# Kernel optimization log

Measured on AMD Instinct MI355X. Metric: run time of the kernel, lower is better.

## Reference

```python
import jax, jax.numpy as jnp
import numpy as np

B, NV, NE = 32, 8192, 65536
SUBSTEPS = 8
DT = 0.01
K_SPRING = 1.0e4   # spring stiffness
CG_ITERS = 20      # fixed CG iterations for the implicit solve
EPS = 1e-12


def setup_inputs() -> dict:
    key = jax.random.key(0)
    k0, k1, k2, k3, k4, k5 = jax.random.split(key, 6)
    # small actuation signals per spring (rest-length modulation)
    input_action = jax.random.normal(k0, (B, NE), dtype=jnp.float32) * 0.05
    # random spring graph with guaranteed i != j
    edge_i = jax.random.randint(k1, (NE,), 0, NV, dtype=jnp.int32)
    off = jax.random.randint(k2, (NE,), 1, NV, dtype=jnp.int32)
    edge_j = ((edge_i + off) % NV).astype(jnp.int32)
    pos0 = jax.random.normal(k3, (B, NV, 3), dtype=jnp.float32) * 0.5
    vel0 = jnp.zeros((B, NV, 3), dtype=jnp.float32)
    # rest lengths near the initial configuration so the system starts close to equilibrium
    d0 = pos0[0, edge_i] - pos0[0, edge_j]
    rest_len = jnp.linalg.norm(d0, axis=-1) + 1e-2
    mass = jax.random.uniform(k4, (NV,), dtype=jnp.float32) + 0.5
    return {"input_action": input_action, "pos0": pos0, "vel0": vel0,
            "rest_len": rest_len, "mass": mass,
            "edge_i": edge_i, "edge_j": edge_j}


def _bdot(a, b):
    # per-batch inner product, keepdims for broadcasting: [B,1,1]
    return jnp.sum(a * b, axis=(1, 2), keepdims=True)


def _spring_force(pos, rest_eff, ei, ej):
    # pos: [B,NV,3], rest_eff: [B,NE]
    d = pos[:, ei] - pos[:, ej]                       # [B,NE,3]
    l = jnp.linalg.norm(d, axis=-1, keepdims=True)    # [B,NE,1]
    dirn = d / jnp.maximum(l, 1e-6)
    fe = -K_SPRING * (l - rest_eff[..., None]) * dirn # [B,NE,3]
    f = jnp.zeros_like(pos).at[:, ei].add(fe).at[:, ej].add(-fe)
    return f


def _matvec(x, mass, ei, ej):
    # A x = M x + dt^2 * k * L x  (graph Laplacian Hessian approximation)
    d = x[:, ei] - x[:, ej]
    Lx = jnp.zeros_like(x).at[:, ei].add(d).at[:, ej].add(-d)
    return mass[None, :, None] * x + (DT * DT * K_SPRING) * Lx


def _cg_solve(b, mass, ei, ej):
    x = jnp.zeros_like(b)
    r = b
    p = r
    rs = _bdot(r, r)

    def body(carry, _):
        x, r, p, rs = carry
        Ap = _matvec(p, mass, ei, ej)
        alpha = rs / (_bdot(p, Ap) + EPS)
        x = x + alpha * p
        r = r - alpha * Ap
        rs_new = _bdot(r, r)
        p = r + (rs_new / (rs + EPS)) * p
        return (x, r, p, rs_new), None

    (x, _, _, _), _ = jax.lax.scan(body, (x, r, p, rs), None, length=CG_ITERS)
    return x


def reference(input_action, pos0, vel0, rest_len, mass, edge_i, edge_j):
    gravity = jnp.array([0.0, -9.8, 0.0], dtype=pos0.dtype)
    rest_eff = rest_len[None, :] * (1.0 + input_action)  # actuated rest lengths [B,NE]
    m3 = mass[None, :, None]

    def step(carry, _):
        pos, vel = carry
        f = _spring_force(pos, rest_eff, edge_i, edge_j) + m3 * gravity
        b = m3 * vel + DT * f                  # implicit Euler RHS
        v_new = _cg_solve(b, mass, edge_i, edge_j)
        pos_new = pos + DT * v_new
        return (pos_new, v_new), pos_new

    _, traj = jax.lax.scan(step, (pos0, vel0), None, length=SUBSTEPS)
    # traj: [SUBSTEPS, B, NV, 3] -> [B, SUBSTEPS, NV, 3]
    return jnp.transpose(traj, (1, 0, 2, 3))
```

## Files before the change

### kernel.cpp

```cpp
#include <hip/hip_runtime.h>
#include <hip/hip_cooperative_groups.h>
#include <math.h>

namespace cg = cooperative_groups;

#define NVERT 8192
#define NEDGE 65536
#define NSUB 8
#define NCG 20
#define GRID 256
#define BLOCK 1024
#define DT 0.01f
#define KS 10000.0f
#define NGRP 16
#define GSIZE 16

struct Params {
  const float* action;
  const float* pos0;
  const float* vel0;
  const float* rest_len;
  const float* mass;
  const int* edge_i;
  const int* edge_j;
  float* out;
  float2* posXY;
  float*  posZ;
  float2 *QXY0, *QXY1;
  float  *QZ0,  *QZ1;
  float* rest_eff;
  int* adj_off;
  int* adjE_off;
  int* row_ptr;
  int* cursor;
  double* Pd;
  double* Gd;
  unsigned* bar;
};

union U64F2 { unsigned long long u; float2 f; };
union U32F  { unsigned u; float f; };
union U64D  { unsigned long long u; double d; };

__device__ __forceinline__ float2 ld2_dev(const float2* p) {
  U64F2 r;
  r.u = __hip_atomic_load((const unsigned long long*)p, __ATOMIC_RELAXED, __HIP_MEMORY_SCOPE_AGENT);
  return r.f;
}
__device__ __forceinline__ void st2_dev(float2* p, float2 v) {
  U64F2 r; r.f = v;
  __hip_atomic_store((unsigned long long*)p, r.u, __ATOMIC_RELAXED, __HIP_MEMORY_SCOPE_AGENT);
}
__device__ __forceinline__ float ldf_dev(const float* p) {
  U32F r;
  r.u = __hip_atomic_load((const unsigned*)p, __ATOMIC_RELAXED, __HIP_MEMORY_SCOPE_AGENT);
  return r.f;
}
__device__ __forceinline__ void stf_dev(float* p, float v) {
  U32F r; r.f = v;
  __hip_atomic_store((unsigned*)p, r.u, __ATOMIC_RELAXED, __HIP_MEMORY_SCOPE_AGENT);
}
__device__ __forceinline__ double lddbl_dev(const double* p) {
  U64D r;
  r.u = __hip_atomic_load((const unsigned long long*)p, __ATOMIC_RELAXED, __HIP_MEMORY_SCOPE_AGENT);
  return r.d;
}
__device__ __forceinline__ void stdbl_dev(double* p, double v) {
  U64D r; r.d = v;
  __hip_atomic_store((unsigned long long*)p, r.u, __ATOMIC_RELAXED, __HIP_MEMORY_SCOPE_AGENT);
}

__device__ __forceinline__ void fast_bar(unsigned* bar, unsigned ep) {
  __syncthreads();
  if (threadIdx.x == 0) {
    const unsigned g = blockIdx.x >> 4;
    const unsigned old = __hip_atomic_fetch_add(bar + g * 32, 1u,
                          __ATOMIC_RELAXED, __HIP_MEMORY_SCOPE_AGENT);
    if (old == GSIZE * ep - 1) {
      const unsigned old2 = __hip_atomic_fetch_add(bar + NGRP * 32, 1u,
                             __ATOMIC_RELAXED, __HIP_MEMORY_SCOPE_AGENT);
      if (old2 == NGRP * ep - 1) {
#pragma unroll
        for (int i = 0; i < NGRP; ++i)
          __hip_atomic_store(bar + (NGRP + 1 + i) * 32, ep,
                             __ATOMIC_RELAXED, __HIP_MEMORY_SCOPE_AGENT);
      }
    }
    while (__hip_atomic_load(bar + (NGRP + 1 + g) * 32,
                             __ATOMIC_RELAXED, __HIP_MEMORY_SCOPE_AGENT) < ep)
      __builtin_amdgcn_s_sleep(1);
  }
  __syncthreads();
}

__device__ __forceinline__ void fast_bar_red(unsigned* bar, unsigned ep,
                                             const double* Pd, double* Gd, int par,
                                             int* lflag) {
  __syncthreads();
  const unsigned g = blockIdx.x >> 4;
  if (threadIdx.x == 0) {
    const unsigned old = __hip_atomic_fetch_add(bar + g * 32, 1u,
                          __ATOMIC_RELAXED, __HIP_MEMORY_SCOPE_AGENT);
    *lflag = (old == GSIZE * ep - 1);
  }
  __syncthreads();
  if (*lflag) {
    if (threadIdx.x < 96) {
      const double* base = Pd + (size_t)par * 256 * 96 + (size_t)(g * GSIZE) * 96
                           + threadIdx.x;
      double s = 0.0;
#pragma unroll
      for (int j = 0; j < GSIZE; ++j) s += lddbl_dev(base + j * 96);
      stdbl_dev(&Gd[(size_t)par * NGRP * 96 + g * 96 + threadIdx.x], s);
    }
    __syncthreads();
    if (threadIdx.x == 0) {
      const unsigned old2 = __hip_atomic_fetch_add(bar + NGRP * 32, 1u,
                             __ATOMIC_RELAXED, __HIP_MEMORY_SCOPE_AGENT);
      if (old2 == NGRP * ep - 1) {
#pragma unroll
        for (int i = 0; i < NGRP; ++i)
          __hip_atomic_store(bar + (NGRP + 1 + i) * 32, ep,
                             __ATOMIC_RELAXED, __HIP_MEMORY_SCOPE_AGENT);
      }
    }
  }
  if (threadIdx.x == 0) {
    while (__hip_atomic_load(bar + (NGRP + 1 + g) * 32,
                             __ATOMIC_RELAXED, __HIP_MEMORY_SCOPE_AGENT) < ep)
      __builtin_amdgcn_s_sleep(1);
  }
  __syncthreads();
}

__device__ __forceinline__ void publish_store(double* Pd, int par, double d0, double d1,
                                              double d2, double* lds) {
  d0 += __shfl_down(d0, 32);
  d1 += __shfl_down(d1, 32);
  d2 += __shfl_down(d2, 32);
  const int lane = threadIdx.x & 63, w = threadIdx.x >> 6;
  if (lane < 32) {
    lds[w * 96 + lane] = d0;
    lds[w * 96 + 32 + lane] = d1;
    lds[w * 96 + 64 + lane] = d2;
  }
  __syncthreads();
  if (threadIdx.x < 96) {
    double s = 0.0;
#pragma unroll
    for (int ww = 0; ww < BLOCK / 64; ++ww) s += lds[ww * 96 + threadIdx.x];
    stdbl_dev(&Pd[(size_t)par * 256 * 96 + (size_t)blockIdx.x * 96 + threadIdx.x], s);
  }
}

__device__ __forceinline__ void reduce_small(const double* Gd, int par,
                                             double* lds_part, double* lds_acc) {
  const int tid = threadIdx.x;
  const double* base = Gd + (size_t)par * NGRP * 96;
  lds_part[tid] = lddbl_dev(base + tid);
  if (tid < NGRP * 96 - BLOCK)
    lds_part[BLOCK + tid] = lddbl_dev(base + BLOCK + tid);
  __syncthreads();
  if (tid < 96) {
    double s = 0.0;
#pragma unroll
    for (int g = 0; g < NGRP; ++g) s += lds_part[g * 96 + tid];
    lds_acc[tid] = s;
  }
  __syncthreads();
}

__global__ void __launch_bounds__(BLOCK) mass_spring_kernel(Params P) {
  cg::grid_group grid = cg::this_grid();
  __shared__ double lds_red[(BLOCK / 64) * 96];
  __shared__ double lds_part[NGRP * 96];
  __shared__ double lds_acc[96];
  __shared__ int lds_scan[BLOCK];
  __shared__ int lds_flag;

  const int tid = threadIdx.x;
  const int gtid = blockIdx.x * BLOCK + tid;
  const int b = tid & 31;
  const int v = gtid >> 5;
  const int vb = v * 32 + b;
  const int b8 = b * 8, b4 = b * 4;
  unsigned ep = 0;

  for (int i = gtid; i < NEDGE * 32; i += GRID * BLOCK) {
    const int e = i >> 5, bb = i & 31;
    P.rest_eff[e * 32 + bb] = P.rest_len[e] * (1.0f + P.action[bb * NEDGE + e]);
  }
  float3 pv, vv;
  pv.x = P.pos0[(b * NVERT + v) * 3 + 0];
  pv.y = P.pos0[(b * NVERT + v) * 3 + 1];
  pv.z = P.pos0[(b * NVERT + v) * 3 + 2];
  vv.x = P.vel0[(b * NVERT + v) * 3 + 0];
  vv.y = P.vel0[(b * NVERT + v) * 3 + 1];
  vv.z = P.vel0[(b * NVERT + v) * 3 + 2];
  st2_dev(&P.posXY[vb], make_float2(pv.x, pv.y));
  stf_dev(&P.posZ[vb], pv.z);
  if (gtid < NVERT) P.cursor[gtid] = 0;
  if (gtid < (2 * NGRP + 1) * 32) P.bar[gtid] = 0u;
  grid.sync();

  if (gtid < NEDGE) {
    atomicAdd(&P.cursor[P.edge_i[gtid]], 1);
    atomicAdd(&P.cursor[P.edge_j[gtid]], 1);
  }
  grid.sync();

  if (blockIdx.x == 0) {
    const int base = tid * (NVERT / BLOCK);
    int loc[NVERT / BLOCK];
    int sum = 0;
#pragma unroll
    for (int i = 0; i < NVERT / BLOCK; ++i) { loc[i] = P.cursor[base + i]; sum += loc[i]; }
    lds_scan[tid] = sum;
    __syncthreads();
    for (int off = 1; off < BLOCK; off <<= 1) {
      int t = 0;
      if (tid >= off) t = lds_scan[tid - off];
      __syncthreads();
      if (tid >= off) lds_scan[tid] += t;
      __syncthreads();
    }
    int run = lds_scan[tid] - sum;
#pragma unroll
    for (int i = 0; i < NVERT / BLOCK; ++i) {
      P.row_ptr[base + i] = run;
      P.cursor[base + i] = run;
      run += loc[i];
    }
    if (tid == BLOCK - 1) P.row_ptr[NVERT] = run;
  }
  grid.sync();

  if (gtid < NEDGE) {
    const int ei = P.edge_i[gtid], ej = P.edge_j[gtid];
    const int ai = atomicAdd(&P.cursor[ei], 1);
    P.adj_off[ai] = ej * 256; P.adjE_off[ai] = gtid * 128;
    const int aj = atomicAdd(&P.cursor[ej], 1);
    P.adj_off[aj] = ei * 256; P.adjE_off[aj] = gtid * 128;
  }
  grid.sync();

  const float m_v = P.mass[v];
  const int rbeg = P.row_ptr[v], rend = P.row_ptr[v + 1];
  const float degf = (float)(rend - rbeg);

  float2* qXYrd = P.QXY0; float2* qXYwr = P.QXY1;
  float*  qZrd  = P.QZ0;  float*  qZwr  = P.QZ1;
  int pub = 0;

  for (int s = 0; s < NSUB; ++s) {
    float fx = 0.f, fy = 0.f, fz = 0.f;
#pragma unroll 4
    for (int a = rbeg; a < rend; ++a) {
      const int off = P.adj_off[a];
      const float2 pxy = ld2_dev((const float2*)((const char*)P.posXY + off + b8));
      const float  puz = ldf_dev((const float*)((const char*)P.posZ + (off >> 1) + b4));
      const float re = *(const float*)((const char*)P.rest_eff + P.adjE_off[a] + b4);
      const float dx = pv.x - pxy.x, dy = pv.y - pxy.y, dz = pv.z - puz;
      const float l = sqrtf(dx * dx + dy * dy + dz * dz);
      const float coef = -KS * (l - re) / fmaxf(l, 1e-6f);
      fx += coef * dx; fy += coef * dy; fz += coef * dz;
    }
    float3 rv;
    rv.x = m_v * vv.x + DT * fx;
    rv.y = m_v * vv.y + DT * (fy - 9.8f * m_v);
    rv.z = m_v * vv.z + DT * fz;
    st2_dev(&qXYrd[vb], make_float2(rv.x, rv.y));
    stf_dev(&qZrd[vb], rv.z);
    float3 xacc = make_float3(0.f, 0.f, 0.f);
    float3 pc = rv;
    float3 ap;
    float3 Sr, Sp;
    fast_bar(P.bar, ++ep);

    for (int k = 0; k < NCG; ++k) {
      if (k == 0) {
        float sx = 0.f, sy = 0.f, sz = 0.f;
#pragma unroll 4
        for (int a = rbeg; a < rend; ++a) {
          const int off = P.adj_off[a];
          const float2 qxy = ld2_dev((const float2*)((const char*)qXYrd + off + b8));
          const float  qz  = ldf_dev((const float*)((const char*)qZrd + (off >> 1) + b4));
          sx += qxy.x; sy += qxy.y; sz += qz;
        }
        Sr = make_float3(sx, sy, sz);
        Sp = Sr;
        ap.x = (m_v + degf) * pc.x - Sp.x;
        ap.y = (m_v + degf) * pc.y - Sp.y;
        ap.z = (m_v + degf) * pc.z - Sp.z;
      } else {
        const double* gbase = P.Gd + (size_t)((pub + 1) & 1) * NGRP * 96;
        const double gval0 = lddbl_dev(gbase + tid);
        double gval1 = 0.0;
        if (tid < NGRP * 96 - BLOCK) gval1 = lddbl_dev(gbase + BLOCK + tid);
        float sx = 0.f, sy = 0.f, sz = 0.f;
#pragma unroll 4
        for (int a = rbeg; a < rend; ++a) {
          const int off = P.adj_off[a];
          const float2 qxy = ld2_dev((const float2*)((const char*)qXYrd + off + b8));
          const float  qz  = ldf_dev((const float*)((const char*)qZrd + (off >> 1) + b4));
          sx += qxy.x; sy += qxy.y; sz += qz;
        }
        lds_part[tid] = gval0;
        if (tid < NGRP * 96 - BLOCK) lds_part[BLOCK + tid] = gval1;
        __syncthreads();
        if (tid < 96) {
          double s = 0.0;
#pragma unroll
          for (int g = 0; g < NGRP; ++g) s += lds_part[g * 96 + tid];
          lds_acc[tid] = s;
        }
        __syncthreads();
        const double rsx = lds_acc[b];
        const double pq  = lds_acc[32 + b];
        const double qq  = lds_acc[64 + b];
        const float alpha = (float)(rsx / (pq + 1e-12));
        const double rs_rec = (double)alpha * (double)alpha * qq - rsx;
        const float beta = (float)(rs_rec / (rsx + 1e-12));
        xacc.x += alpha * pc.x; xacc.y += alpha * pc.y; xacc.z += alpha * pc.z;
        rv.x -= alpha * ap.x; rv.y -= alpha * ap.y; rv.z -= alpha * ap.z;
        Sr.x -= alpha * sx; Sr.y -= alpha * sy; Sr.z -= alpha * sz;
        pc.x = rv.x + beta * pc.x; pc.y = rv.y + beta * pc.y; pc.z = rv.z + beta * pc.z;
        Sp.x = Sr.x + beta * Sp.x; Sp.y = Sr.y + beta * Sp.y; Sp.z = Sr.z + beta * Sp.z;
        ap.x = (m_v + degf) * pc.x - Sp.x;
        ap.y = (m_v + degf) * pc.y - Sp.y;
        ap.z = (m_v + degf) * pc.z - Sp.z;
      }
      st2_dev(&qXYwr[vb], make_float2(ap.x, ap.y));
      stf_dev(&qZwr[vb], ap.z);
      publish_store(P.Pd, pub & 1,
                    (double)(rv.x * rv.x) + (double)(rv.y * rv.y) + (double)(rv.z * rv.z),
                    (double)(pc.x * ap.x) + (double)(pc.y * ap.y) + (double)(pc.z * ap.z),
                    (double)(ap.x * ap.x) + (double)(ap.y * ap.y) + (double)(ap.z * ap.z),
                    lds_red);
      fast_bar_red(P.bar, ++ep, P.Pd, P.Gd, pub & 1, &lds_flag);
      ++pub;
      float2* t2 = qXYrd; qXYrd = qXYwr; qXYwr = t2;
      float*  t1 = qZrd;  qZrd  = qZwr;  qZwr  = t1;
    }

    {
      reduce_small(P.Gd, (pub + 1) & 1, lds_part, lds_acc);
      const double rsx = lds_acc[b];
      const double pq  = lds_acc[32 + b];
      const float alpha = (float)(rsx / (pq + 1e-12));
      xacc.x += alpha * pc.x; xacc.y += alpha * pc.y; xacc.z += alpha * pc.z;
      vv = xacc;
      pv.x += DT * vv.x; pv.y += DT * vv.y; pv.z += DT * vv.z;
      st2_dev(&P.posXY[vb], make_float2(pv.x, pv.y));
      stf_dev(&P.posZ[vb], pv.z);
      float* o = P.out + ((size_t)(b * NSUB + s) * NVERT + (size_t)v) * 3;
      o[0] = pv.x; o[1] = pv.y; o[2] = pv.z;
      fast_bar(P.bar, ++ep);
    }
  }
}

extern "C" void kernel_launch(void* const* d_in, const int* in_sizes, int n_in,
                              void* d_out, int out_size, void* d_ws, size_t ws_size,
                              hipStream_t stream) {
  Params P;
  P.action = (const float*)d_in[0];
  P.pos0 = (const float*)d_in[1];
  P.vel0 = (const float*)d_in[2];
  P.rest_len = (const float*)d_in[3];
  P.mass = (const float*)d_in[4];
  P.edge_i = (const int*)d_in[5];
  P.edge_j = (const int*)d_in[6];
  P.out = (float*)d_out;

  char* w = (char*)d_ws;
  auto alloc = [&](size_t bytes) {
    char* p = w;
    w += (bytes + 255) & ~(size_t)255;
    return p;
  };
  const size_t xy_bytes = (size_t)NVERT * 32 * sizeof(float2);
  const size_t z_bytes  = (size_t)NVERT * 32 * sizeof(float);
  P.posXY = (float2*)alloc(xy_bytes);
  P.posZ  = (float*)alloc(z_bytes);
  P.QXY0  = (float2*)alloc(xy_bytes);
  P.QXY1  = (float2*)alloc(xy_bytes);
  P.QZ0   = (float*)alloc(z_bytes);
  P.QZ1   = (float*)alloc(z_bytes);
  P.rest_eff = (float*)alloc((size_t)NEDGE * 32 * sizeof(float));
  P.adj_off  = (int*)alloc((size_t)2 * NEDGE * sizeof(int));
  P.adjE_off = (int*)alloc((size_t)2 * NEDGE * sizeof(int));
  P.row_ptr  = (int*)alloc((size_t)(NVERT + 1) * sizeof(int));
  P.cursor   = (int*)alloc((size_t)NVERT * sizeof(int));
  P.Pd       = (double*)alloc((size_t)2 * 256 * 96 * sizeof(double));
  P.Gd       = (double*)alloc((size_t)2 * NGRP * 96 * sizeof(double));
  P.bar      = (unsigned*)alloc((size_t)(2 * NGRP + 1) * 32 * sizeof(unsigned));

  void* args[] = { &P };
  hipLaunchCooperativeKernel(reinterpret_cast<void*>(mass_spring_kernel),
                             dim3(GRID), dim3(BLOCK), args, 0, stream);
}
```

Measured before the change: 2.086 ms.

## Replace two-level barrier with flat per-group counter polling; skip last-iteration stores

The grid barrier changes from a hierarchical scheme, where the last block of a group bumps a top counter and a final block broadcasts release flags, to one where every block adds to its group counter and polls all 16 group counters. In the reduction barrier each group leader sets its own flag and all blocks poll the 16 flags. This removes one serial atomic hop from the barrier critical path, in exchange for more polling loads per block. Separately, the q-vector stores on the final CG iteration are skipped because nothing reads them.

After: 2.089 ms (median of 2 runs). About the same (+0.2%).

```diff
diff --git a/kernel.cpp b/kernel.cpp
--- a/kernel.cpp
+++ b/kernel.cpp
@@ -74,21 +74,18 @@
   __syncthreads();
   if (threadIdx.x == 0) {
     const unsigned g = blockIdx.x >> 4;
-    const unsigned old = __hip_atomic_fetch_add(bar + g * 32, 1u,
-                          __ATOMIC_RELAXED, __HIP_MEMORY_SCOPE_AGENT);
-    if (old == GSIZE * ep - 1) {
-      const unsigned old2 = __hip_atomic_fetch_add(bar + NGRP * 32, 1u,
-                             __ATOMIC_RELAXED, __HIP_MEMORY_SCOPE_AGENT);
-      if (old2 == NGRP * ep - 1) {
-#pragma unroll
-        for (int i = 0; i < NGRP; ++i)
-          __hip_atomic_store(bar + (NGRP + 1 + i) * 32, ep,
-                             __ATOMIC_RELAXED, __HIP_MEMORY_SCOPE_AGENT);
-      }
-    }
-    while (__hip_atomic_load(bar + (NGRP + 1 + g) * 32,
-                             __ATOMIC_RELAXED, __HIP_MEMORY_SCOPE_AGENT) < ep)
+    __hip_atomic_fetch_add(bar + g * 32, 1u,
+                           __ATOMIC_RELAXED, __HIP_MEMORY_SCOPE_AGENT);
+    const unsigned tgt = GSIZE * ep;
+    for (;;) {
+      bool ok = true;
+#pragma unroll
+      for (int i = 0; i < NGRP; ++i)
+        ok &= (__hip_atomic_load(bar + i * 32,
+                                 __ATOMIC_RELAXED, __HIP_MEMORY_SCOPE_AGENT) >= tgt);
+      if (ok) break;
       __builtin_amdgcn_s_sleep(1);
+    }
   }
   __syncthreads();
 }
@@ -114,21 +111,20 @@
       stdbl_dev(&Gd[(size_t)par * NGRP * 96 + g * 96 + threadIdx.x], s);
     }
     __syncthreads();
-    if (threadIdx.x == 0) {
-      const unsigned old2 = __hip_atomic_fetch_add(bar + NGRP * 32, 1u,
-                             __ATOMIC_RELAXED, __HIP_MEMORY_SCOPE_AGENT);
-      if (old2 == NGRP * ep - 1) {
-#pragma unroll
-        for (int i = 0; i < NGRP; ++i)
-          __hip_atomic_store(bar + (NGRP + 1 + i) * 32, ep,
-                             __ATOMIC_RELAXED, __HIP_MEMORY_SCOPE_AGENT);
-      }
-    }
+    if (threadIdx.x == 0)
+      __hip_atomic_store(bar + (NGRP + 1 + g) * 32, ep,
+                         __ATOMIC_RELAXED, __HIP_MEMORY_SCOPE_AGENT);
   }
   if (threadIdx.x == 0) {
-    while (__hip_atomic_load(bar + (NGRP + 1 + g) * 32,
-                             __ATOMIC_RELAXED, __HIP_MEMORY_SCOPE_AGENT) < ep)
+    for (;;) {
+      bool ok = true;
+#pragma unroll
+      for (int i = 0; i < NGRP; ++i)
+        ok &= (__hip_atomic_load(bar + (NGRP + 1 + i) * 32,
+                                 __ATOMIC_RELAXED, __HIP_MEMORY_SCOPE_AGENT) >= ep);
+      if (ok) break;
       __builtin_amdgcn_s_sleep(1);
+    }
   }
   __syncthreads();
 }
@@ -330,8 +326,10 @@
         ap.y = (m_v + degf) * pc.y - Sp.y;
         ap.z = (m_v + degf) * pc.z - Sp.z;
       }
-      st2_dev(&qXYwr[vb], make_float2(ap.x, ap.y));
-      stf_dev(&qZwr[vb], ap.z);
+      if (k != NCG - 1) {
+        st2_dev(&qXYwr[vb], make_float2(ap.x, ap.y));
+        stf_dev(&qZwr[vb], ap.z);
+      }
       publish_store(P.Pd, pub & 1,
                     (double)(rv.x * rv.x) + (double)(rv.y * rv.y) + (double)(rv.z * rv.z),
                     (double)(pc.x * ap.x) + (double)(pc.y * ap.y) + (double)(pc.z * ap.z),
```
